# Performance work log

Measured on AMD Instinct MI355X. Metric: run time of the kernel, lower is better.

The kernel has to match this reference:

```python
import jax, jax.numpy as jnp
import numpy as np

NET_W, NET_H = 416, 416
ALL_ANCHORS = np.array([10,13, 16,30, 33,23, 30,61, 62,45, 59,119, 116,90, 156,198, 373,326], dtype=np.float32).reshape(-1, 2)
ANCH13 = jnp.asarray(ALL_ANCHORS[[6, 7, 8]])  # stride-32 head
ANCH26 = jnp.asarray(ALL_ANCHORS[[3, 4, 5]])  # stride-16 head
ANCH52 = jnp.asarray(ALL_ANCHORS[[0, 1, 2]])  # stride-8 head
NUM_CLASSES = 80


def head_conv(f, W, b):
    # 1x1 conv, linear activation, with bias (yolo head conv has no BN)
    return jnp.einsum('bchw,oc->bohw', f, W) + b[None, :, None, None]


def yolo_decode(p, anchors):
    # Faithful vectorization of Yolov3Layer.forward + get_yolo_boxes
    B, C, H, W = p.shape
    A = anchors.shape[0]
    attrs = C // A  # 5 + classes
    pr = jnp.transpose(p.reshape(B, A, attrs, H, W), (0, 1, 3, 4, 2))  # (B,A,H,W,attrs)
    sx = jax.nn.sigmoid(pr[..., 0])
    sy = jax.nn.sigmoid(pr[..., 1])
    tw = pr[..., 2]
    th = pr[..., 3]
    conf = jax.nn.sigmoid(pr[..., 4])
    cls = jax.nn.sigmoid(pr[..., 5:])
    col = jnp.arange(W, dtype=p.dtype)[None, None, None, :]
    row = jnp.arange(H, dtype=p.dtype)[None, None, :, None]
    # source uses grid_w = shape[2] (=H) and grid_h = shape[3] (=W); grids are square so H==W
    bx = (col + sx) / W
    by = (row + sy) / H
    bw = jnp.exp(tw) * anchors[:, 0][None, :, None, None] / NET_W
    bh = jnp.exp(th) * anchors[:, 1][None, :, None, None] / NET_H
    boxes = jnp.stack([bx, by, bw, bh], axis=-1)  # (B,A,H,W,4)
    return jnp.concatenate([
        boxes.reshape(B, -1, 4),
        conf.reshape(B, -1, 1),
        cls.reshape(B, -1, NUM_CLASSES),
    ], axis=-1)  # (B, A*H*W, 85)


def setup_inputs() -> dict:
    key = jax.random.key(0)
    ks = jax.random.split(key, 6)
    f13 = jax.random.normal(ks[0], (32, 1024, 13, 13), dtype=jnp.float32)
    f26 = jax.random.normal(ks[1], (32, 512, 26, 26), dtype=jnp.float32)
    f52 = jax.random.normal(ks[2], (32, 256, 52, 52), dtype=jnp.float32)
    # fan-in scaled weights so head outputs are ~N(0,1) and exp() stays bounded
    W13 = jax.random.normal(ks[3], (255, 1024), dtype=jnp.float32) / np.sqrt(1024.0)
    W26 = jax.random.normal(ks[4], (255, 512), dtype=jnp.float32) / np.sqrt(512.0)
    W52 = jax.random.normal(ks[5], (255, 256), dtype=jnp.float32) / np.sqrt(256.0)
    b13 = jnp.zeros((255,), jnp.float32)
    b26 = jnp.zeros((255,), jnp.float32)
    b52 = jnp.zeros((255,), jnp.float32)
    return {"f13": f13, "f26": f26, "f52": f52, "W13": W13, "b13": b13,
            "W26": W26, "b26": b26, "W52": W52, "b52": b52}


def reference(f13, f26, f52, W13, b13, W26, b26, W52, b52):
    out13 = yolo_decode(head_conv(f13, W13, b13), ANCH13)
    out26 = yolo_decode(head_conv(f26, W26, b26), ANCH26)
    out52 = yolo_decode(head_conv(f52, W52, b52), ANCH52)
    return (out13, out26, out52)
```

## Files before the change

kernel.cpp:

```cpp
#include <hip/hip_runtime.h>
#include <hip/hip_bf16.h>
#include <stdint.h>

typedef float  f32x4  __attribute__((ext_vector_type(4)));
typedef float  f32x2  __attribute__((ext_vector_type(2)));
typedef short  s16x8  __attribute__((ext_vector_type(8)));
typedef unsigned short u16;

#define DEVI __device__ __forceinline__

DEVI u16 f2bf(float x) {
  union { __hip_bfloat16 b; u16 u; } c;
  c.b = __float2bfloat16(x);
  return c.u;
}
DEVI float bf2f(u16 h) { return __uint_as_float(((uint32_t)h) << 16); }

DEVI int unperm(int pr) {
  if (pr < 6) return 85 * (pr >> 1) + 2 + (pr & 1);
  int idx = pr - 6;
  return idx + (idx < 2 ? 0 : (idx < 85 ? 2 : (idx < 168 ? 4 : 6)));
}

template<int HEAD> DEVI float anchW(int a) {
  if constexpr (HEAD == 0) return a == 0 ? 116.f/416.f : (a == 1 ? 156.f/416.f : 373.f/416.f);
  else if constexpr (HEAD == 1) return a == 0 ? 30.f/416.f : (a == 1 ? 62.f/416.f : 59.f/416.f);
  else return a == 0 ? 10.f/416.f : (a == 1 ? 16.f/416.f : 33.f/416.f);
}
template<int HEAD> DEVI float anchH(int a) {
  if constexpr (HEAD == 0) return a == 0 ? 90.f/416.f : (a == 1 ? 198.f/416.f : 326.f/416.f);
  else if constexpr (HEAD == 1) return a == 0 ? 61.f/416.f : (a == 1 ? 45.f/416.f : 119.f/416.f);
  else return a == 0 ? 13.f/416.f : (a == 1 ? 30.f/416.f : 23.f/416.f);
}

template<int K, int LOGK>
DEVI void pack_head(const float* __restrict__ Wt, u16* __restrict__ dst,
                    int i, int alBaseWords) {
  const int pr = i >> LOGK;
  const int k  = i & (K - 1);
  float x = 0.f;
  if (pr < 255) x = Wt[(size_t)unperm(pr) * K + k];
  const u16 hi = f2bf(x);
  const int t    = k >> 5;
  const int rb   = pr >> 4;
  const int lane = (pr & 15) | (((k >> 3) & 3) << 4);
  const int elem = k & 7;
  dst[((size_t)(t * 16 + rb)) * 512 + lane * 8 + elem] = hi;
  if (pr < 16)
    dst[(size_t)alBaseWords + (size_t)t * 512 + lane * 8 + elem] = f2bf(x - bf2f(hi));
}

__global__ __launch_bounds__(256)
void pack_all(const float* __restrict__ W13, const float* __restrict__ W26,
              const float* __restrict__ W52, u16* __restrict__ p13,
              u16* __restrict__ p26, u16* __restrict__ p52) {
  const int g = (int)(blockIdx.x * 256 + threadIdx.x);
  if (g < 262144)       pack_head<1024, 10>(W13, p13, g,            262144);
  else if (g < 393216)  pack_head< 512,  9>(W26, p26, g - 262144,   131072);
  else                  pack_head< 256,  8>(W52, p52, g - 393216,    65536);
}

struct Shm {
  float raw[256 * 17];
  float bias[256];
  u16   perm[256];
  f32x2 cw[16];
};

template<int K, int WD, int HEAD>
DEVI void head_block(const float* __restrict__ F, const u16* __restrict__ Wp,
                     const float* __restrict__ bias_g, float* __restrict__ out,
                     int bidx, Shm* sh)
{
  constexpr int S  = WD * WD;
  constexpr int NT = (S + 15) / 16;
  constexpr int NSTEP = K / 32;
  constexpr float invWD = 1.f / (float)WD;

  const int b  = bidx / NT;
  const int s0 = (bidx - b * NT) * 16;
  const int tid  = (int)threadIdx.x;
  const int lane = tid & 63;
  const int wmu  = (int)__builtin_amdgcn_readfirstlane((unsigned)(tid >> 6));
  const int ridx = lane & 15;
  const int g8   = (lane >> 4) << 3;

  {
    const int m_of = unperm(tid);
    sh->perm[m_of] = (u16)tid;
    sh->bias[tid] = (tid < 255) ? bias_g[m_of] : 0.f;
    if (tid < 16) {
      int s = s0 + tid; if (s >= S) s = S - 1;
      const int hh = s / WD;
      const int ww = s - hh * WD;
      sh->cw[tid] = f32x2{(float)ww * invWD, (float)hh * invWD};
    }
  }

  const float* Fb = F + (size_t)b * K * S;
  const int bc   = s0 + ridx;
  const int bcol = bc < S ? bc : S - 1;
  int boff[8];
  #pragma unroll
  for (int e = 0; e < 8; ++e) boff[e] = (g8 + e) * S + bcol;

  const u16* Abase  = Wp + (size_t)wmu * 4 * 512 + lane * 8;
  const u16* Albase = Wp + (size_t)K * 256 + lane * 8;

  f32x4 acc[4];
  #pragma unroll
  for (int i = 0; i < 4; ++i)
    #pragma unroll
    for (int r = 0; r < 4; ++r) acc[i][r] = 0.f;

  s16x8 A[4], Alo;
  float B0[8], B1[8];

#define LOADA(tt) do {                                                        \
    const u16* ap_ = Abase + (size_t)(tt) * 16 * 512;                         \
    A[0] = *(const s16x8*)(ap_);                                              \
    A[1] = *(const s16x8*)(ap_ + 512);                                        \
    A[2] = *(const s16x8*)(ap_ + 1024);                                       \
    A[3] = *(const s16x8*)(ap_ + 1536);                                       \
    if (wmu == 0) Alo = *(const s16x8*)(Albase + (size_t)(tt) * 512);         \
  } while (0)

#define LOADB(Bx, tt) do {                                                    \
    const float* fp_ = Fb + (size_t)(tt) * 32 * S;                            \
    _Pragma("unroll")                                                         \
    for (int e_ = 0; e_ < 8; ++e_) Bx[e_] = fp_[boff[e_]];                    \
  } while (0)

#define COMPUTE(Bx) do {                                                      \
    u16 bh_[8]; s16x8 Bh_;                                                    \
    _Pragma("unroll")                                                         \
    for (int e_ = 0; e_ < 8; ++e_) { bh_[e_] = f2bf(Bx[e_]); Bh_[e_] = (short)bh_[e_]; } \
    _Pragma("unroll")                                                         \
    for (int mf_ = 0; mf_ < 4; ++mf_)                                         \
      acc[mf_] = __builtin_amdgcn_mfma_f32_16x16x32_bf16(A[mf_], Bh_, acc[mf_], 0, 0, 0); \
    if (wmu == 0) {                                                           \
      s16x8 Bl_;                                                              \
      _Pragma("unroll")                                                       \
      for (int e_ = 0; e_ < 8; ++e_) Bl_[e_] = (short)f2bf(Bx[e_] - bf2f(bh_[e_])); \
      acc[0] = __builtin_amdgcn_mfma_f32_16x16x32_bf16(A[0], Bl_, acc[0], 0, 0, 0); \
      acc[0] = __builtin_amdgcn_mfma_f32_16x16x32_bf16(Alo, Bh_, acc[0], 0, 0, 0); \
    }                                                                         \
  } while (0)

  LOADB(B0, 0);
  LOADB(B1, 1);
  for (int t = 0; t < NSTEP; t += 2) {
    LOADA(t);
    COMPUTE(B0);
    if (t + 2 < NSTEP) LOADB(B0, t + 2);
    LOADA(t + 1);
    COMPUTE(B1);
    if (t + 3 < NSTEP) LOADB(B1, t + 3);
  }

#undef LOADA
#undef LOADB
#undef COMPUTE

  #pragma unroll
  for (int mf = 0; mf < 4; ++mf)
    #pragma unroll
    for (int r = 0; r < 4; ++r) {
      const int pr = wmu * 64 + mf * 16 + ((lane >> 4) << 2) + r;
      sh->raw[pr * 17 + ridx] = acc[mf][r] + sh->bias[pr];
    }
  __syncthreads();

  const int vs = (S - s0) < 16 ? (S - s0) : 16;
  const int sq0 = tid / 85;
  const int at0 = tid - 85 * sq0;
  #pragma unroll
  for (int a = 0; a < 3; ++a) {
    const float aw = anchW<HEAD>(a);
    const float ah = anchH<HEAD>(a);
    float* oa = out + ((size_t)(b * 3 + a) * S + s0) * 85;
    int i = tid, at = at0, sq = sq0;
    #pragma unroll
    for (int j = 0; j < 6; ++j) {
      if (i < 1360 && sq < vs) {
        const int pr  = (int)sh->perm[a * 85 + at];
        const float p = sh->raw[pr * 17 + sq];
        const float e  = __expf(p);
        const float sg = e * __builtin_amdgcn_rcpf(e + 1.f);
        const f32x2 c  = sh->cw[sq];
        float val;
        if      (at == 0) val = fmaf(sg, invWD, c[0]);
        else if (at == 1) val = fmaf(sg, invWD, c[1]);
        else if (at == 2) val = e * aw;
        else if (at == 3) val = e * ah;
        else              val = sg;
        oa[i] = val;
      }
      i += 256; at += 1; sq += 3;
      if (at >= 85) { at -= 85; sq += 1; }
    }
  }
}

__global__ __launch_bounds__(256, 6)
void yolo_fused(const float* __restrict__ f13, const float* __restrict__ f26,
                const float* __restrict__ f52,
                const u16* __restrict__ p13, const float* __restrict__ b13,
                const u16* __restrict__ p26, const float* __restrict__ b26,
                const u16* __restrict__ p52, const float* __restrict__ b52,
                float* __restrict__ out)
{
  __shared__ Shm sh;
  const int blk = (int)blockIdx.x;
  float* out13 = out;
  float* out26 = out + 1379040;
  float* out52 = out + 6895200;
  if (blk < 352)        head_block<1024, 13, 0>(f13, p13, b13, out13, blk,        &sh);
  else if (blk < 1728)  head_block< 512, 26, 1>(f26, p26, b26, out26, blk - 352,  &sh);
  else                  head_block< 256, 52, 2>(f52, p52, b52, out52, blk - 1728, &sh);
}

extern "C" void kernel_launch(void* const* d_in, const int* in_sizes, int n_in,
                              void* d_out, int out_size, void* d_ws, size_t ws_size,
                              hipStream_t stream) {
  (void)in_sizes; (void)n_in; (void)ws_size; (void)out_size;
  const float* f13 = (const float*)d_in[0];
  const float* f26 = (const float*)d_in[1];
  const float* f52 = (const float*)d_in[2];
  const float* W13 = (const float*)d_in[3];
  const float* b13 = (const float*)d_in[4];
  const float* W26 = (const float*)d_in[5];
  const float* b26 = (const float*)d_in[6];
  const float* W52 = (const float*)d_in[7];
  const float* b52 = (const float*)d_in[8];

  u16* p13 = (u16*)d_ws;
  u16* p26 = p13 + 278528;
  u16* p52 = p26 + 139264;

  pack_all<<<dim3(1792), dim3(256), 0, stream>>>(W13, W26, W52, p13, p26, p52);
  yolo_fused<<<dim3(7136), dim3(256), 0, stream>>>(
      f13, f26, f52, p13, b13, p26, b26, p52, b52, (float*)d_out);
}
```

Baseline: 124.5 us.

## Deepen B prefetch to four buffers and remap block-to-tile order for XCD locality

The K-loop now keeps four register buffers of feature values in flight instead of two, so more global loads overlap the MFMA work. Occupancy is lowered from 6 to 5 waves per SIMD to make room for the extra registers. Block indices are also permuted so that consecutive tiles land on the same XCD (blk&7 selects a contiguous chunk), which should improve L2 reuse of neighbouring feature columns. The cost is fewer resident waves and more register pressure. The loop also assumes NSTEP is a multiple of 4.

```diff
diff --git a/kernel.cpp b/kernel.cpp
--- a/kernel.cpp
+++ b/kernel.cpp
@@ -114,7 +114,7 @@
     for (int r = 0; r < 4; ++r) acc[i][r] = 0.f;
 
   s16x8 A[4], Alo;
-  float B0[8], B1[8];
+  float B0[8], B1[8], B2[8], B3[8];
 
 #define LOADA(tt) do {                                                        \
     const u16* ap_ = Abase + (size_t)(tt) * 16 * 512;                         \
@@ -147,15 +147,12 @@
     }                                                                         \
   } while (0)
 
-  LOADB(B0, 0);
-  LOADB(B1, 1);
-  for (int t = 0; t < NSTEP; t += 2) {
-    LOADA(t);
-    COMPUTE(B0);
-    if (t + 2 < NSTEP) LOADB(B0, t + 2);
-    LOADA(t + 1);
-    COMPUTE(B1);
-    if (t + 3 < NSTEP) LOADB(B1, t + 3);
+  LOADB(B0, 0); LOADB(B1, 1); LOADB(B2, 2); LOADB(B3, 3);
+  for (int t = 0; t < NSTEP; t += 4) {
+    LOADA(t);     COMPUTE(B0); if (t + 4 < NSTEP) LOADB(B0, t + 4);
+    LOADA(t + 1); COMPUTE(B1); if (t + 5 < NSTEP) LOADB(B1, t + 5);
+    LOADA(t + 2); COMPUTE(B2); if (t + 6 < NSTEP) LOADB(B2, t + 6);
+    LOADA(t + 3); COMPUTE(B3); if (t + 7 < NSTEP) LOADB(B3, t + 7);
   }
 
 #undef LOADA
@@ -202,7 +199,7 @@
   }
 }
 
-__global__ __launch_bounds__(256, 6)
+__global__ __launch_bounds__(256, 5)
 void yolo_fused(const float* __restrict__ f13, const float* __restrict__ f26,
                 const float* __restrict__ f52,
                 const u16* __restrict__ p13, const float* __restrict__ b13,
@@ -215,9 +212,18 @@
   float* out13 = out;
   float* out26 = out + 1379040;
   float* out52 = out + 6895200;
-  if (blk < 352)        head_block<1024, 13, 0>(f13, p13, b13, out13, blk,        &sh);
-  else if (blk < 1728)  head_block< 512, 26, 1>(f26, p26, b26, out26, blk - 352,  &sh);
-  else                  head_block< 256, 52, 2>(f52, p52, b52, out52, blk - 1728, &sh);
+  if (blk < 352) {
+    const int tile = (blk & 7) * 44 + (blk >> 3);
+    head_block<1024, 13, 0>(f13, p13, b13, out13, tile, &sh);
+  } else if (blk < 1728) {
+    const int i = blk - 352;
+    const int tile = (i & 7) * 172 + (i >> 3);
+    head_block< 512, 26, 1>(f26, p26, b26, out26, tile, &sh);
+  } else {
+    const int i = blk - 1728;
+    const int tile = (i & 7) * 676 + (i >> 3);
+    head_block< 256, 52, 2>(f52, p52, b52, out52, tile, &sh);
+  }
 }
 
 extern "C" void kernel_launch(void* const* d_in, const int* in_sizes, int n_in,
```

New measurement: 271.3 us. 118% more time.
